# Kernel optimization log

Hardware: AMD Instinct MI355X
Metric: run time of the kernel (lower is better)

The kernel has to match this reference:

```python
import jax, jax.numpy as jnp
import numpy as np

N_NODES = 100000
N_EDGES = 1600000
IN_DIM, H1, H2, OUT_DIM = 128, 64, 32, 16


def setup_inputs() -> dict:
    key = jax.random.key(0)
    ks = jax.random.split(key, 9)
    x = jax.random.normal(ks[0], (N_NODES, IN_DIM), dtype=jnp.float32)
    edge_index = jax.random.randint(ks[1], (2, N_EDGES), 0, N_NODES, dtype=jnp.int64)
    # nn.Linear-style params (out_feats, in_feats) + bias
    def lin(k, o, i):
        bound = 1.0 / np.sqrt(i)
        kw, kb = jax.random.split(k)
        W = jax.random.uniform(kw, (o, i), jnp.float32, -bound, bound)
        b = jax.random.uniform(kb, (o,), jnp.float32, -bound, bound)
        return W, b
    W1, b1 = lin(ks[2], H1, IN_DIM)
    W2, b2 = lin(ks[3], H2, H1)
    Wf, bf = lin(ks[4], OUT_DIM, H2)
    return {"x": x, "edge_index": edge_index, "W1": W1, "b1": b1,
            "W2": W2, "b2": b2, "Wf": Wf, "bf": bf}


def reference(x, edge_index, W1, b1, W2, b2, Wf, bf):
    # Original: adj = to_dense_adj(edge_index); graph built from adj.T; DGL
    # copy_src+sum then gives new_h[src] = sum over dst of h[dst], i.e. A @ h
    # with A[src, dst]. No activation between layers (unused in forward),
    # dropout inactive at inference.
    N = x.shape[0]
    src, dst = edge_index[0], edge_index[1]

    def aggregate(h):  # sum of out-neighbor features: [N, d]
        return jax.ops.segment_sum(h[dst], src, num_segments=N)

    h = aggregate(x) @ W1.T + b1          # [N, 64]
    h = aggregate(h) @ W2.T + b2          # [N, 32]
    pooled = jnp.max(h, axis=0)           # [32] global max pool over nodes
    return pooled @ Wf.T + bf             # [16]
```

## Files before the change

kernel.cpp:

```cpp
#include <hip/hip_runtime.h>

#define N_NODES 100000
#define N_EDGES 1600000
#define IN_DIM 128
#define H1_DIM 64
#define H2_DIM 32
#define OUT_DIM 16

#define NPB 64
#define KB 1563
#define OFFW (KB + 1)
#define NCH 256
#define CH_E (N_EDGES / NCH)
#define CAP2 1536
#define NBIN1 64
#define NBIN2 (NCH - NBIN1)
#define NGB 782

typedef __attribute__((ext_vector_type(8))) short short8;
typedef __attribute__((ext_vector_type(4))) float f32x4;

__device__ inline unsigned short f2b(float v) {
    unsigned u = __float_as_uint(v);
    u += 0x7FFF + ((u >> 16) & 1);
    return (unsigned short)(u >> 16);
}
__device__ inline short f2bs(float v) { return (short)f2b(v); }
__device__ inline unsigned f32_to_key(float v) {
    unsigned u = __float_as_uint(v);
    return (v >= 0.f) ? (u | 0x80000000u) : ~u;
}
__device__ __forceinline__ void acc8(float* a, uint4 v) {
    a[0] += __uint_as_float(v.x << 16);
    a[1] += __uint_as_float(v.x & 0xFFFF0000u);
    a[2] += __uint_as_float(v.y << 16);
    a[3] += __uint_as_float(v.y & 0xFFFF0000u);
    a[4] += __uint_as_float(v.z << 16);
    a[5] += __uint_as_float(v.z & 0xFFFF0000u);
    a[6] += __uint_as_float(v.w << 16);
    a[7] += __uint_as_float(v.w & 0xFFFF0000u);
}

__device__ __forceinline__ void bin_chunk(const int* __restrict__ src,
                                          const int* __restrict__ dst,
                                          unsigned* __restrict__ off,
                                          unsigned* __restrict__ grec, int c) {
    __shared__ int hist[2048];
    __shared__ int part[512];
    __shared__ int cur[2048];
    int t = threadIdx.x;
    int e0 = c * CH_E;
    for (int i = t; i < 2048; i += 512) hist[i] = 0;
    __syncthreads();
    for (int e = t; e < CH_E; e += 512) atomicAdd(&hist[src[e0 + e] >> 6], 1);
    __syncthreads();
    int h0 = hist[4 * t], h1 = hist[4 * t + 1], h2 = hist[4 * t + 2], h3 = hist[4 * t + 3];
    int tot = h0 + h1 + h2 + h3;
    part[t] = tot;
    __syncthreads();
    for (int o = 1; o < 512; o <<= 1) {
        int a = (t >= o) ? part[t - o] : 0;
        __syncthreads();
        part[t] += a;
        __syncthreads();
    }
    int gb = part[t] - tot;
    int o0 = gb, o1 = gb + h0, o2 = o1 + h1, o3 = o2 + h2;
    int b4 = 4 * t;
    cur[b4] = o0; cur[b4 + 1] = o1; cur[b4 + 2] = o2; cur[b4 + 3] = o3;
    if (b4 + 0 < KB) off[(size_t)c * OFFW + b4 + 0] = o0;
    if (b4 + 1 < KB) off[(size_t)c * OFFW + b4 + 1] = o1;
    if (b4 + 2 < KB) off[(size_t)c * OFFW + b4 + 2] = o2;
    if (b4 + 3 < KB) off[(size_t)c * OFFW + b4 + 3] = o3;
    if (t == 0) off[(size_t)c * OFFW + KB] = CH_E;
    __syncthreads();
    for (int e = t; e < CH_E; e += 512) {
        int s = src[e0 + e];
        int d = dst[e0 + e];
        int p = atomicAdd(&cur[s >> 6], 1);
        grec[(size_t)e0 + p] = ((unsigned)(s & 63) << 17) | (unsigned)d;
    }
}

__global__ __launch_bounds__(512) void k1_kernel(const int* __restrict__ src,
                                                 const int* __restrict__ dst,
                                                 unsigned* __restrict__ off,
                                                 unsigned* __restrict__ grec,
                                                 const float* __restrict__ W1,
                                                 const float* __restrict__ W2,
                                                 unsigned short* __restrict__ Wcb) {
    if (blockIdx.x < NBIN1) {
        bin_chunk(src, dst, off, grec, blockIdx.x);
        return;
    }
    int t = threadIdx.x;
    for (int idx = t; idx < H2_DIM * IN_DIM; idx += 512) {
        int j = idx >> 7, f = idx & 127;
        float acc = 0.f;
        for (int k = 0; k < H1_DIM; ++k)
            acc += W2[j * H1_DIM + k] * W1[k * IN_DIM + f];
        Wcb[idx] = f2b(acc);
    }
}

__global__ __launch_bounds__(512) void k2_kernel(const int* __restrict__ src,
                                                 const int* __restrict__ dst,
                                                 unsigned* __restrict__ off,
                                                 unsigned* __restrict__ grec,
                                                 const float* __restrict__ x,
                                                 const unsigned short* __restrict__ Wcb,
                                                 unsigned short* __restrict__ yb) {
    if (blockIdx.x < NBIN2) {
        bin_chunk(src, dst, off, grec, NBIN1 + blockIdx.x);
        return;
    }
    int gb = blockIdx.x - NBIN2;
    int t = threadIdx.x;
    int w = t >> 6, l = t & 63;
    int row = l & 15, kg = l >> 4;
    int base = gb * 128 + w * 16;
    int node = base + row;
    int nclamp = (node < N_NODES) ? node : (N_NODES - 1);
    const float* xp = x + (size_t)nclamp * IN_DIM + kg * 8;
    const unsigned short* b0p = Wcb + (size_t)row * IN_DIM + kg * 8;
    const unsigned short* b1p = Wcb + (size_t)(16 + row) * IN_DIM + kg * 8;
    f32x4 acc0 = {0.f, 0.f, 0.f, 0.f}, acc1 = {0.f, 0.f, 0.f, 0.f};
#pragma unroll
    for (int kk = 0; kk < 4; ++kk) {
        float4 xa = *(const float4*)(xp + kk * 32);
        float4 xb = *(const float4*)(xp + kk * 32 + 4);
        short8 a;
        a[0] = f2bs(xa.x); a[1] = f2bs(xa.y); a[2] = f2bs(xa.z); a[3] = f2bs(xa.w);
        a[4] = f2bs(xb.x); a[5] = f2bs(xb.y); a[6] = f2bs(xb.z); a[7] = f2bs(xb.w);
        short8 b0 = *(const short8*)(b0p + kk * 32);
        short8 b1 = *(const short8*)(b1p + kk * 32);
        acc0 = __builtin_amdgcn_mfma_f32_16x16x32_bf16(a, b0, acc0, 0, 0, 0);
        acc1 = __builtin_amdgcn_mfma_f32_16x16x32_bf16(a, b1, acc1, 0, 0, 0);
    }
#pragma unroll
    for (int r = 0; r < 4; ++r) {
        int n2 = base + kg * 4 + r;
        if (n2 < N_NODES) {
            yb[(size_t)n2 * H2_DIM + row]      = f2b(acc0[r]);
            yb[(size_t)n2 * H2_DIM + 16 + row] = f2b(acc1[r]);
        }
    }
}

template <int ROUND>
__global__ __launch_bounds__(512) void agg_kernel(const unsigned short* __restrict__ in,
                                                  const unsigned* __restrict__ off,
                                                  const unsigned* __restrict__ grec,
                                                  unsigned* __restrict__ grec2,
                                                  unsigned* __restrict__ noff,
                                                  unsigned short* __restrict__ z1b,
                                                  const float* __restrict__ W2,
                                                  const float* __restrict__ b1,
                                                  const float* __restrict__ b2,
                                                  unsigned* __restrict__ pk) {
    __shared__ int len[NCH], pos[NCH], sst[NCH];
    __shared__ int shist[64], scur2[64];
    __shared__ int sscan[65];
    __shared__ unsigned rbuf[CAP2];
    __shared__ unsigned sbuf[CAP2];
    __shared__ float smq[32][4][8];
    __shared__ float scv[32], sb2v[32];
    __shared__ int s_cnt;
    int t = threadIdx.x;
    int b = blockIdx.x;
    int gid = t >> 4;
    int L = t & 15;
    int chunk = L & 3, subset = L >> 2;

    if (ROUND == 1) {
        if (t < NCH) {
            unsigned o0 = off[(size_t)t * OFFW + b];
            unsigned o1 = off[(size_t)t * OFFW + b + 1];
            sst[t] = (int)o0;
            len[t] = (int)(o1 - o0);
            pos[t] = (int)(o1 - o0);
        }
        __syncthreads();
        for (int o = 1; o < NCH; o <<= 1) {
            int a = (t < NCH && t >= o) ? pos[t - o] : 0;
            __syncthreads();
            if (t < NCH) pos[t] += a;
            __syncthreads();
        }
        if (t < NCH) pos[t] -= len[t];
        if (t == NCH - 1) s_cnt = min(pos[t] + len[t], CAP2);
        __syncthreads();
        for (int c = gid; c < NCH; c += 32) {
            int Ln = len[c], P = pos[c], S = sst[c];
            for (int k = L; k < Ln; k += 16) {
                int q = P + k;
                if (q < CAP2) rbuf[q] = grec[(size_t)c * CH_E + S + k];
            }
        }
        if (t < 64) shist[t] = 0;
        __syncthreads();
        int cnt = s_cnt;
        for (int i = t; i < cnt; i += 512) atomicAdd(&shist[rbuf[i] >> 17], 1);
        __syncthreads();
        if (t < 64) scur2[t] = shist[t];
        __syncthreads();
        for (int o = 1; o < 64; o <<= 1) {
            int a = (t < 64 && t >= o) ? scur2[t - o] : 0;
            __syncthreads();
            if (t < 64) scur2[t] += a;
            __syncthreads();
        }
        if (t < 64) sscan[t] = scur2[t] - shist[t];
        if (t == 63) sscan[64] = scur2[63];
        __syncthreads();
        if (t < 64) scur2[t] = sscan[t];
        __syncthreads();
        for (int i = t; i < cnt; i += 512) {
            unsigned r = rbuf[i];
            int p = atomicAdd(&scur2[r >> 17], 1);
            if (p < CAP2) sbuf[p] = r;
        }
        __syncthreads();
        for (int i = t; i < cnt; i += 512) grec2[(size_t)b * CAP2 + i] = sbuf[i];
        if (t < 65) noff[(size_t)b * 65 + t] = (unsigned)sscan[t];
    } else {
        if (t < 65) sscan[t] = (int)noff[(size_t)b * 65 + t];
        __syncthreads();
        int cnt = sscan[64];
        for (int i = t; i < cnt; i += 512) sbuf[i] = grec2[(size_t)b * CAP2 + i];
        if (t < 32) {
            float s = 0.f;
            for (int k = 0; k < H1_DIM; ++k) s += W2[t * H1_DIM + k] * b1[k];
            scv[t] = s;
            sb2v[t] = b2[t];
        }
    }
    __syncthreads();

    float cfv[8], bbv[8], m[8];
    if (ROUND == 2) {
#pragma unroll
        for (int j = 0; j < 8; ++j) {
            cfv[j] = scv[chunk * 8 + j];
            bbv[j] = sb2v[chunk * 8 + j];
            m[j] = -3.402823466e+38f;
        }
    }

    for (int sl = gid; sl < NPB; sl += 32) {
        int r0 = sscan[sl], r1 = sscan[sl + 1];
        float a[8] = {0.f, 0.f, 0.f, 0.f, 0.f, 0.f, 0.f, 0.f};
        float aa[8] = {0.f, 0.f, 0.f, 0.f, 0.f, 0.f, 0.f, 0.f};
        for (int e = r0; e < r1; e += 8) {
            int eA = e + subset, eB = e + 4 + subset;
            if (eA < r1) {
                unsigned rc = sbuf[eA];
                uint4 v = *(const uint4*)(in + (size_t)(rc & 0x1FFFFu) * H2_DIM + chunk * 8);
                acc8(a, v);
            }
            if (eB < r1) {
                unsigned rc = sbuf[eB];
                uint4 v = *(const uint4*)(in + (size_t)(rc & 0x1FFFFu) * H2_DIM + chunk * 8);
                acc8(aa, v);
            }
        }
#pragma unroll
        for (int j = 0; j < 8; ++j) {
            float s = a[j] + aa[j];
            s += __shfl_xor(s, 4);
            s += __shfl_xor(s, 8);
            a[j] = s;
        }
        int node = b * NPB + sl;
        if (node < N_NODES) {
            if (ROUND == 1) {
                if (subset == 0) {
                    uint4 o;
                    o.x = (unsigned)f2b(a[0]) | ((unsigned)f2b(a[1]) << 16);
                    o.y = (unsigned)f2b(a[2]) | ((unsigned)f2b(a[3]) << 16);
                    o.z = (unsigned)f2b(a[4]) | ((unsigned)f2b(a[5]) << 16);
                    o.w = (unsigned)f2b(a[6]) | ((unsigned)f2b(a[7]) << 16);
                    *(uint4*)(z1b + (size_t)node * H2_DIM + chunk * 8) = o;
                }
            } else {
                float dg = (float)(r1 - r0);
#pragma unroll
                for (int j = 0; j < 8; ++j)
                    m[j] = fmaxf(m[j], a[j] + dg * cfv[j] + bbv[j]);
            }
        }
    }
    if (ROUND == 2) {
        if (subset == 0) {
#pragma unroll
            for (int j = 0; j < 8; ++j) smq[gid][chunk][j] = m[j];
        }
        __syncthreads();
        if (t < 32) {
            int c = t >> 3, j = t & 7;
            float mm = smq[0][c][j];
#pragma unroll
            for (int k = 1; k < 32; ++k) mm = fmaxf(mm, smq[k][c][j]);
            atomicMax(&pk[t], f32_to_key(mm));
        }
    }
}

__global__ void final_kernel(const unsigned* __restrict__ pk,
                             const float* __restrict__ Wf,
                             const float* __restrict__ bfv,
                             float* __restrict__ out) {
    __shared__ float pooled[H2_DIM];
    int t = threadIdx.x;
    if (t < H2_DIM) {
        unsigned k = pk[t];
        unsigned u = (k & 0x80000000u) ? (k & 0x7FFFFFFFu) : ~k;
        pooled[t] = __uint_as_float(u);
    }
    __syncthreads();
    if (t < OUT_DIM) {
        float acc = bfv[t];
        for (int j = 0; j < H2_DIM; ++j)
            acc += Wf[t * H2_DIM + j] * pooled[j];
        out[t] = acc;
    }
}

extern "C" void kernel_launch(void* const* d_in, const int* in_sizes, int n_in,
                              void* d_out, int out_size, void* d_ws, size_t ws_size,
                              hipStream_t stream) {
    const float* x  = (const float*)d_in[0];
    const int*   ei = (const int*)d_in[1];
    const float* W1 = (const float*)d_in[2];
    const float* b1 = (const float*)d_in[3];
    const float* W2 = (const float*)d_in[4];
    const float* b2 = (const float*)d_in[5];
    const float* Wf = (const float*)d_in[6];
    const float* bf = (const float*)d_in[7];
    float* out = (float*)d_out;

    const int* src = ei;
    const int* dst = ei + N_EDGES;

    unsigned short* yb  = (unsigned short*)d_ws;
    unsigned short* z1b = yb + (size_t)N_NODES * H2_DIM;
    unsigned short* Wcb = z1b + (size_t)N_NODES * H2_DIM;
    unsigned* pk    = (unsigned*)(Wcb + H2_DIM * IN_DIM);
    unsigned* off   = pk + H2_DIM;
    unsigned* grec  = off + (size_t)NCH * OFFW;
    unsigned* grec2 = grec + N_EDGES;
    unsigned* noff  = grec2 + (size_t)KB * CAP2;

    hipMemsetAsync(pk, 0, H2_DIM * sizeof(unsigned), stream);

    k1_kernel<<<NBIN1 + 1, 512, 0, stream>>>(src, dst, off, grec, W1, W2, Wcb);
    k2_kernel<<<NBIN2 + NGB, 512, 0, stream>>>(src, dst, off, grec, x, Wcb, yb);

    agg_kernel<1><<<KB, 512, 0, stream>>>(yb, off, grec, grec2, noff, z1b,
                                          nullptr, nullptr, nullptr, pk);
    agg_kernel<2><<<KB, 512, 0, stream>>>(z1b, off, grec, grec2, noff, nullptr,
                                          W2, b1, b2, pk);

    final_kernel<<<1, 64, 0, stream>>>(pk, Wf, bf, out);
}
```

Before: 125.4 us.

## Split aggregation into specialized kernels, binary-search gather, and one-node-per-group second round

The templated aggregation kernel is split into two dedicated kernels. In the first round, gathering bucketed records no longer walks each of 256 chunks with a 16-lane group. Each thread now binary-searches the prefix array for its flat index, which balances the gather across all threads. The second round uses 1024-thread blocks with one 16-lane group per node and no shared-memory staging of records. The W2·b1 bias vector is precomputed once in k1 rather than in every block. These changes aim to cut load imbalance, shared-memory traffic and per-block setup, at the cost of larger blocks that may lower occupancy flexibility.

```diff
diff --git a/kernel.cpp b/kernel.cpp
--- a/kernel.cpp
+++ b/kernel.cpp
@@ -87,8 +87,10 @@
                                                  unsigned* __restrict__ off,
                                                  unsigned* __restrict__ grec,
                                                  const float* __restrict__ W1,
+                                                 const float* __restrict__ b1,
                                                  const float* __restrict__ W2,
-                                                 unsigned short* __restrict__ Wcb) {
+                                                 unsigned short* __restrict__ Wcb,
+                                                 float* __restrict__ cvb) {
     if (blockIdx.x < NBIN1) {
         bin_chunk(src, dst, off, grec, blockIdx.x);
         return;
@@ -100,6 +102,11 @@
         for (int k = 0; k < H1_DIM; ++k)
             acc += W2[j * H1_DIM + k] * W1[k * IN_DIM + f];
         Wcb[idx] = f2b(acc);
+    }
+    if (t < H2_DIM) {
+        float s = 0.f;
+        for (int k = 0; k < H1_DIM; ++k) s += W2[t * H1_DIM + k] * b1[k];
+        cvb[t] = s;
     }
 }
 
@@ -147,24 +154,17 @@
     }
 }
 
-template <int ROUND>
-__global__ __launch_bounds__(512) void agg_kernel(const unsigned short* __restrict__ in,
-                                                  const unsigned* __restrict__ off,
-                                                  const unsigned* __restrict__ grec,
-                                                  unsigned* __restrict__ grec2,
-                                                  unsigned* __restrict__ noff,
-                                                  unsigned short* __restrict__ z1b,
-                                                  const float* __restrict__ W2,
-                                                  const float* __restrict__ b1,
-                                                  const float* __restrict__ b2,
-                                                  unsigned* __restrict__ pk) {
-    __shared__ int len[NCH], pos[NCH], sst[NCH];
+__global__ __launch_bounds__(512) void agg1_kernel(const unsigned short* __restrict__ in,
+                                                   const unsigned* __restrict__ off,
+                                                   const unsigned* __restrict__ grec,
+                                                   unsigned* __restrict__ grec2,
+                                                   unsigned* __restrict__ noff,
+                                                   unsigned short* __restrict__ z1b) {
+    __shared__ int pos[NCH + 1], sst[NCH], len[NCH];
     __shared__ int shist[64], scur2[64];
     __shared__ int sscan[65];
     __shared__ unsigned rbuf[CAP2];
     __shared__ unsigned sbuf[CAP2];
-    __shared__ float smq[32][4][8];
-    __shared__ float scv[32], sb2v[32];
     __shared__ int s_cnt;
     int t = threadIdx.x;
     int b = blockIdx.x;
@@ -172,80 +172,62 @@
     int L = t & 15;
     int chunk = L & 3, subset = L >> 2;
 
-    if (ROUND == 1) {
-        if (t < NCH) {
-            unsigned o0 = off[(size_t)t * OFFW + b];
-            unsigned o1 = off[(size_t)t * OFFW + b + 1];
-            sst[t] = (int)o0;
-            len[t] = (int)(o1 - o0);
-            pos[t] = (int)(o1 - o0);
-        }
-        __syncthreads();
-        for (int o = 1; o < NCH; o <<= 1) {
-            int a = (t < NCH && t >= o) ? pos[t - o] : 0;
-            __syncthreads();
-            if (t < NCH) pos[t] += a;
-            __syncthreads();
-        }
-        if (t < NCH) pos[t] -= len[t];
-        if (t == NCH - 1) s_cnt = min(pos[t] + len[t], CAP2);
-        __syncthreads();
-        for (int c = gid; c < NCH; c += 32) {
-            int Ln = len[c], P = pos[c], S = sst[c];
-            for (int k = L; k < Ln; k += 16) {
-                int q = P + k;
-                if (q < CAP2) rbuf[q] = grec[(size_t)c * CH_E + S + k];
-            }
-        }
-        if (t < 64) shist[t] = 0;
-        __syncthreads();
-        int cnt = s_cnt;
-        for (int i = t; i < cnt; i += 512) atomicAdd(&shist[rbuf[i] >> 17], 1);
-        __syncthreads();
-        if (t < 64) scur2[t] = shist[t];
-        __syncthreads();
-        for (int o = 1; o < 64; o <<= 1) {
-            int a = (t < 64 && t >= o) ? scur2[t - o] : 0;
-            __syncthreads();
-            if (t < 64) scur2[t] += a;
-            __syncthreads();
-        }
-        if (t < 64) sscan[t] = scur2[t] - shist[t];
-        if (t == 63) sscan[64] = scur2[63];
-        __syncthreads();
-        if (t < 64) scur2[t] = sscan[t];
-        __syncthreads();
-        for (int i = t; i < cnt; i += 512) {
-            unsigned r = rbuf[i];
-            int p = atomicAdd(&scur2[r >> 17], 1);
-            if (p < CAP2) sbuf[p] = r;
-        }
-        __syncthreads();
-        for (int i = t; i < cnt; i += 512) grec2[(size_t)b * CAP2 + i] = sbuf[i];
-        if (t < 65) noff[(size_t)b * 65 + t] = (unsigned)sscan[t];
-    } else {
-        if (t < 65) sscan[t] = (int)noff[(size_t)b * 65 + t];
-        __syncthreads();
-        int cnt = sscan[64];
-        for (int i = t; i < cnt; i += 512) sbuf[i] = grec2[(size_t)b * CAP2 + i];
-        if (t < 32) {
-            float s = 0.f;
-            for (int k = 0; k < H1_DIM; ++k) s += W2[t * H1_DIM + k] * b1[k];
-            scv[t] = s;
-            sb2v[t] = b2[t];
-        }
-    }
-    __syncthreads();
-
-    float cfv[8], bbv[8], m[8];
-    if (ROUND == 2) {
-#pragma unroll
-        for (int j = 0; j < 8; ++j) {
-            cfv[j] = scv[chunk * 8 + j];
-            bbv[j] = sb2v[chunk * 8 + j];
-            m[j] = -3.402823466e+38f;
-        }
-    }
+    if (t < NCH) {
+        unsigned o0 = off[(size_t)t * OFFW + b];
+        unsigned o1 = off[(size_t)t * OFFW + b + 1];
+        sst[t] = (int)o0;
+        len[t] = (int)(o1 - o0);
+        pos[t] = (int)(o1 - o0);
+    }
+    __syncthreads();
+    for (int o = 1; o < NCH; o <<= 1) {
+        int a = (t < NCH && t >= o) ? pos[t - o] : 0;
+        __syncthreads();
+        if (t < NCH) pos[t] += a;
+        __syncthreads();
+    }
+    if (t < NCH) pos[t] -= len[t];
+    if (t == NCH - 1) {
+        pos[NCH] = pos[t] + len[t];
+        s_cnt = min(pos[t] + len[t], CAP2);
+    }
+    __syncthreads();
+    int cnt = s_cnt;
+    for (int i = t; i < cnt; i += 512) {
+        int lo = 0, hi = NCH;
+#pragma unroll
+        for (int s = 0; s < 8; ++s) {
+            int mid = (lo + hi) >> 1;
+            if (pos[mid] <= i) lo = mid; else hi = mid;
+        }
+        rbuf[i] = grec[(size_t)lo * CH_E + sst[lo] + (i - pos[lo])];
+    }
+    if (t < 64) shist[t] = 0;
+    __syncthreads();
+    for (int i = t; i < cnt; i += 512) atomicAdd(&shist[rbuf[i] >> 17], 1);
+    __syncthreads();
+    if (t < 64) scur2[t] = shist[t];
+    __syncthreads();
+    for (int o = 1; o < 64; o <<= 1) {
+        int a = (t < 64 && t >= o) ? scur2[t - o] : 0;
+        __syncthreads();
+        if (t < 64) scur2[t] += a;
+        __syncthreads();
+    }
+    if (t < 64) sscan[t] = scur2[t] - shist[t];
+    if (t == 63) sscan[64] = scur2[63];
+    __syncthreads();
+    if (t < 64) scur2[t] = sscan[t];
+    __syncthreads();
+    for (int i = t; i < cnt; i += 512) {
+        unsigned r = rbuf[i];
+        int p = atomicAdd(&scur2[r >> 17], 1);
+        if (p < CAP2) sbuf[p] = r;
+    }
+    __syncthreads();
+    for (int i = t; i < cnt; i += 512) grec2[(size_t)b * CAP2 + i] = sbuf[i];
+    if (t < 65) noff[(size_t)b * 65 + t] = (unsigned)sscan[t];
+    __syncthreads();
 
     for (int sl = gid; sl < NPB; sl += 32) {
         int r0 = sscan[sl], r1 = sscan[sl + 1];
@@ -272,37 +254,76 @@
             a[j] = s;
         }
         int node = b * NPB + sl;
-        if (node < N_NODES) {
-            if (ROUND == 1) {
-                if (subset == 0) {
-                    uint4 o;
-                    o.x = (unsigned)f2b(a[0]) | ((unsigned)f2b(a[1]) << 16);
-                    o.y = (unsigned)f2b(a[2]) | ((unsigned)f2b(a[3]) << 16);
-                    o.z = (unsigned)f2b(a[4]) | ((unsigned)f2b(a[5]) << 16);
-                    o.w = (unsigned)f2b(a[6]) | ((unsigned)f2b(a[7]) << 16);
-                    *(uint4*)(z1b + (size_t)node * H2_DIM + chunk * 8) = o;
-                }
-            } else {
-                float dg = (float)(r1 - r0);
-#pragma unroll
-                for (int j = 0; j < 8; ++j)
-                    m[j] = fmaxf(m[j], a[j] + dg * cfv[j] + bbv[j]);
-            }
-        }
-    }
-    if (ROUND == 2) {
-        if (subset == 0) {
-#pragma unroll
-            for (int j = 0; j < 8; ++j) smq[gid][chunk][j] = m[j];
-        }
-        __syncthreads();
-        if (t < 32) {
-            int c = t >> 3, j = t & 7;
-            float mm = smq[0][c][j];
-#pragma unroll
-            for (int k = 1; k < 32; ++k) mm = fmaxf(mm, smq[k][c][j]);
-            atomicMax(&pk[t], f32_to_key(mm));
-        }
+        if (node < N_NODES && subset == 0) {
+            uint4 o;
+            o.x = (unsigned)f2b(a[0]) | ((unsigned)f2b(a[1]) << 16);
+            o.y = (unsigned)f2b(a[2]) | ((unsigned)f2b(a[3]) << 16);
+            o.z = (unsigned)f2b(a[4]) | ((unsigned)f2b(a[5]) << 16);
+            o.w = (unsigned)f2b(a[6]) | ((unsigned)f2b(a[7]) << 16);
+            *(uint4*)(z1b + (size_t)node * H2_DIM + chunk * 8) = o;
+        }
+    }
+}
+
+__global__ __launch_bounds__(1024) void agg2_kernel(const unsigned short* __restrict__ in,
+                                                    const unsigned* __restrict__ grec2,
+                                                    const unsigned* __restrict__ noff,
+                                                    const float* __restrict__ cvb,
+                                                    const float* __restrict__ b2,
+                                                    unsigned* __restrict__ pk) {
+    __shared__ float smq[64][4][8];
+    int t = threadIdx.x;
+    int b = blockIdx.x;
+    int gid = t >> 4;
+    int L = t & 15;
+    int chunk = L & 3, subset = L >> 2;
+
+    int r0 = (int)noff[(size_t)b * 65 + gid];
+    int r1 = (int)noff[(size_t)b * 65 + gid + 1];
+    const unsigned* rp = grec2 + (size_t)b * CAP2;
+
+    float a[8] = {0.f, 0.f, 0.f, 0.f, 0.f, 0.f, 0.f, 0.f};
+    float aa[8] = {0.f, 0.f, 0.f, 0.f, 0.f, 0.f, 0.f, 0.f};
+    for (int e = r0; e < r1; e += 8) {
+        int eA = e + subset, eB = e + 4 + subset;
+        if (eA < r1) {
+            unsigned rc = rp[eA];
+            uint4 v = *(const uint4*)(in + (size_t)(rc & 0x1FFFFu) * H2_DIM + chunk * 8);
+            acc8(a, v);
+        }
+        if (eB < r1) {
+            unsigned rc = rp[eB];
+            uint4 v = *(const uint4*)(in + (size_t)(rc & 0x1FFFFu) * H2_DIM + chunk * 8);
+            acc8(aa, v);
+        }
+    }
+#pragma unroll
+    for (int j = 0; j < 8; ++j) {
+        float s = a[j] + aa[j];
+        s += __shfl_xor(s, 4);
+        s += __shfl_xor(s, 8);
+        a[j] = s;
+    }
+
+    int node = b * NPB + gid;
+    float m[8];
+    float dg = (float)(r1 - r0);
+#pragma unroll
+    for (int j = 0; j < 8; ++j) {
+        float v = a[j] + dg * cvb[chunk * 8 + j] + b2[chunk * 8 + j];
+        m[j] = (node < N_NODES) ? v : -3.402823466e+38f;
+    }
+    if (subset == 0) {
+#pragma unroll
+        for (int j = 0; j < 8; ++j) smq[gid][chunk][j] = m[j];
+    }
+    __syncthreads();
+    if (t < 32) {
+        int c = t >> 3, j = t & 7;
+        float mm = smq[0][c][j];
+#pragma unroll
+        for (int k = 1; k < 64; ++k) mm = fmaxf(mm, smq[k][c][j]);
+        atomicMax(&pk[t], f32_to_key(mm));
     }
 }
 
@@ -345,7 +366,8 @@
     unsigned short* yb  = (unsigned short*)d_ws;
     unsigned short* z1b = yb + (size_t)N_NODES * H2_DIM;
     unsigned short* Wcb = z1b + (size_t)N_NODES * H2_DIM;
-    unsigned* pk    = (unsigned*)(Wcb + H2_DIM * IN_DIM);
+    float* cvb      = (float*)(Wcb + H2_DIM * IN_DIM);
+    unsigned* pk    = (unsigned*)(cvb + H2_DIM);
     unsigned* off   = pk + H2_DIM;
     unsigned* grec  = off + (size_t)NCH * OFFW;
     unsigned* grec2 = grec + N_EDGES;
@@ -353,13 +375,11 @@
 
     hipMemsetAsync(pk, 0, H2_DIM * sizeof(unsigned), stream);
 
-    k1_kernel<<<NBIN1 + 1, 512, 0, stream>>>(src, dst, off, grec, W1, W2, Wcb);
+    k1_kernel<<<NBIN1 + 1, 512, 0, stream>>>(src, dst, off, grec, W1, b1, W2, Wcb, cvb);
     k2_kernel<<<NBIN2 + NGB, 512, 0, stream>>>(src, dst, off, grec, x, Wcb, yb);
 
-    agg_kernel<1><<<KB, 512, 0, stream>>>(yb, off, grec, grec2, noff, z1b,
-                                          nullptr, nullptr, nullptr, pk);
-    agg_kernel<2><<<KB, 512, 0, stream>>>(z1b, off, grec, grec2, noff, nullptr,
-                                          W2, b1, b2, pk);
+    agg1_kernel<<<KB, 512, 0, stream>>>(yb, off, grec, grec2, noff, z1b);
+    agg2_kernel<<<KB, 1024, 0, stream>>>(z1b, grec2, noff, cvb, b2, pk);
 
     final_kernel<<<1, 64, 0, stream>>>(pk, Wf, bf, out);
 }
```

After: 120.6 us. 3.8% less time.
